# Optimization experiments

Hardware: AMD Instinct MI355X
Metric: run time of the kernel (lower is better)

## Reference

```python
import jax, jax.numpy as jnp
import numpy as np

B, IN, H = 8192, 1024, 1024

def setup_inputs() -> dict:
    key = jax.random.key(0)
    ks = jax.random.split(key, 11)
    s = 1.0 / np.sqrt(IN + H)  # torch Linear default init range
    def W(k):
        return jax.random.uniform(k, (H, IN + H), jnp.float32, -s, s)
    def b(k):
        return jax.random.uniform(k, (H,), jnp.float32, -s, s)
    return {
        "inputs": jax.random.normal(ks[0], (B, IN), jnp.float32),
        "hidden": jax.random.normal(ks[1], (B, H), jnp.float32),
        "c": jax.random.normal(ks[2], (B, H), jnp.float32),
        "Wf": W(ks[3]), "bf": b(ks[4]),
        "Wi": W(ks[5]), "bi": b(ks[6]),
        "Wo": W(ks[7]), "bo": b(ks[8]),
        "Wc": W(ks[9]), "bc": b(ks[10]),
    }

def reference(inputs, hidden, c, Wf, bf, Wi, bi, Wo, bo, Wc, bc):
    # concat order matches torch: [hidden, inputs]
    x = jnp.concatenate([hidden, inputs], axis=1)  # [B, H+IN]
    # fuse the four gate linears into one GEMM: [B, H+IN] x [H+IN, 4H]
    Wall = jnp.concatenate([Wf, Wi, Wo, Wc], axis=0)  # [4H, H+IN]
    ball = jnp.concatenate([bf, bi, bo, bc], axis=0)  # [4H]
    gates = x @ Wall.T + ball                         # [B, 4H]
    f, i, o, c_hat = jnp.split(gates, 4, axis=1)
    f = jax.nn.sigmoid(f)
    i = jax.nn.sigmoid(i)
    o = jax.nn.sigmoid(o)
    c_hat = jnp.tanh(c_hat)
    c_new = f * c + i * c_hat
    h_new = o * jnp.tanh(c_new)
    return (h_new, c_new)
```

## Files before the change

### kernel.cpp

```cpp
#include <hip/hip_runtime.h>
#include <cstdint>

#define Bdim 8192
#define Hdim 1024
#define Kdim 2048
#define BM 128
#define BU 64

#define XELEMS ((size_t)Bdim * Kdim)
#define WELEMS ((size_t)4 * Hdim * Kdim)
#define WGATE  ((size_t)Hdim * Kdim)

typedef __bf16 bf16;
typedef bf16  bf16x8   __attribute__((ext_vector_type(8)));
typedef float floatx16 __attribute__((ext_vector_type(16)));

typedef __attribute__((address_space(1))) uint32_t gu32;
typedef __attribute__((address_space(3))) uint32_t lu32;

__device__ __forceinline__ void gl_lds16(const bf16* g, bf16* l) {
    __builtin_amdgcn_global_load_lds((gu32*)(bf16*)g, (lu32*)l, 16, 0, 0);
}

__device__ __forceinline__ float sigf(float x) {
    return 1.0f / (1.0f + __expf(-x));
}
__device__ __forceinline__ float tanhfast(float x) {
    return 2.0f / (1.0f + __expf(-2.0f * x)) - 1.0f;
}

__global__ __launch_bounds__(256) void cvt_kernel(
    const float* __restrict__ inp, const float* __restrict__ hid,
    const float* __restrict__ Wf,  const float* __restrict__ Wi,
    const float* __restrict__ Wo,  const float* __restrict__ Wc,
    bf16* __restrict__ xc, bf16* __restrict__ wc)
{
    const size_t id = (size_t)blockIdx.x * 256 + threadIdx.x;
    const size_t e  = id * 8;
    const float* src;
    bf16* dst;
    if (e < XELEMS) {
        const size_t b = e >> 11;
        const size_t k = e & (Kdim - 1);
        src = (k < Hdim) ? (hid + b * Hdim + k) : (inp + b * Hdim + (k - Hdim));
        dst = xc + e;
    } else {
        const size_t w = e - XELEMS;
        const size_t g = w >> 21;
        const float* Ws = (g == 0) ? Wf : (g == 1) ? Wi : (g == 2) ? Wo : Wc;
        src = Ws + (w & (WGATE - 1));
        dst = wc + w;
    }
    const float4 a  = *reinterpret_cast<const float4*>(src);
    const float4 b4 = *reinterpret_cast<const float4*>(src + 4);
    bf16x8 o;
    o[0] = (bf16)a.x;  o[1] = (bf16)a.y;  o[2] = (bf16)a.z;  o[3] = (bf16)a.w;
    o[4] = (bf16)b4.x; o[5] = (bf16)b4.y; o[6] = (bf16)b4.z; o[7] = (bf16)b4.w;
    *reinterpret_cast<bf16x8*>(dst) = o;
}

__global__ __launch_bounds__(256, 2) void lstm_fused(
    const bf16* __restrict__ xc,   const bf16* __restrict__ wc,
    const float* __restrict__ cin,
    const float* __restrict__ bfv, const float* __restrict__ biv,
    const float* __restrict__ bov, const float* __restrict__ bcv,
    float* __restrict__ out)
{
    __shared__ __align__(16) bf16 As[2 * BM * 32];
    __shared__ __align__(16) bf16 Bs[2 * 4 * BU * 32];

    const int tid  = threadIdx.x;
    const int lane = tid & 63;
    const int wv   = tid >> 6;
    const int m31  = lane & 31;
    const int h32  = lane >> 5;

    const int m0 = blockIdx.x * BM;
    const int u0 = blockIdx.y * BU;

    const bf16* gA[2];
    bf16* lA[2];
    #pragma unroll
    for (int c = 0; c < 2; ++c) {
        const int li   = c * 256 + tid;
        const int row  = li >> 2;
        const int slot = li & 3;
        const int gch  = slot ^ ((row >> 1) & 3);
        gA[c] = xc + (size_t)(m0 + row) * Kdim + gch * 8;
        lA[c] = &As[li * 8];
    }
    const bf16* gB[4];
    bf16* lB[4];
    #pragma unroll
    for (int c = 0; c < 4; ++c) {
        const int li   = c * 256 + tid;
        const int nr   = li >> 2;
        const int slot = li & 3;
        const int gch  = slot ^ ((nr >> 1) & 3);
        const int g    = nr >> 6;
        const int ul   = nr & 63;
        gB[c] = wc + (size_t)g * WGATE + (size_t)(u0 + ul) * Kdim + gch * 8;
        lB[c] = &Bs[li * 8];
    }

    const int rbase = (wv & 1) * 64;
    const int ubase = (wv >> 1) * 32;
    int aoff[2][2];
    #pragma unroll
    for (int a = 0; a < 2; ++a) {
        const int ra = rbase + a * 32 + m31;
        const int t  = (ra >> 1) & 3;
        #pragma unroll
        for (int ks = 0; ks < 2; ++ks)
            aoff[a][ks] = ra * 32 + (((ks * 2 + h32) ^ t) * 8);
    }
    int boff[4][2];
    #pragma unroll
    for (int g = 0; g < 4; ++g) {
        const int rb = g * 64 + ubase + m31;
        const int t  = (rb >> 1) & 3;
        #pragma unroll
        for (int ks = 0; ks < 2; ++ks)
            boff[g][ks] = rb * 32 + (((ks * 2 + h32) ^ t) * 8);
    }

    floatx16 acc[2][4] = {};

    for (int k0 = 0; k0 < Kdim; k0 += 64) {
        #pragma unroll
        for (int s = 0; s < 2; ++s) {
            const int kk = k0 + s * 32;
            gl_lds16(gA[0] + kk, lA[0] + s * (BM * 32));
            gl_lds16(gA[1] + kk, lA[1] + s * (BM * 32));
            gl_lds16(gB[0] + kk, lB[0] + s * (4 * BU * 32));
            gl_lds16(gB[1] + kk, lB[1] + s * (4 * BU * 32));
            gl_lds16(gB[2] + kk, lB[2] + s * (4 * BU * 32));
            gl_lds16(gB[3] + kk, lB[3] + s * (4 * BU * 32));
        }
        __syncthreads();

        #pragma unroll
        for (int s = 0; s < 2; ++s) {
            const bf16* Ab = As + s * (BM * 32);
            const bf16* Bb = Bs + s * (4 * BU * 32);
            bf16x8 af[2][2];
            #pragma unroll
            for (int a = 0; a < 2; ++a)
                #pragma unroll
                for (int ks = 0; ks < 2; ++ks)
                    af[a][ks] = *reinterpret_cast<const bf16x8*>(Ab + aoff[a][ks]);
            bf16x8 bg[4][2];
            #pragma unroll
            for (int g = 0; g < 4; ++g)
                #pragma unroll
                for (int ks = 0; ks < 2; ++ks)
                    bg[g][ks] = *reinterpret_cast<const bf16x8*>(Bb + boff[g][ks]);

            #pragma unroll
            for (int ks = 0; ks < 2; ++ks)
                #pragma unroll
                for (int a = 0; a < 2; ++a)
                    #pragma unroll
                    for (int g = 0; g < 4; ++g)
                        acc[a][g] = __builtin_amdgcn_mfma_f32_32x32x16_bf16(
                            af[a][ks], bg[g][ks], acc[a][g], 0, 0, 0);
        }
        __syncthreads();
    }

    const int m_base = m0 + rbase + 4 * h32;
    const int unit   = u0 + ubase + m31;
    const float bff = bfv[unit];
    const float bii = biv[unit];
    const float boo = bov[unit];
    const float bcc = bcv[unit];
    #pragma unroll
    for (int a = 0; a < 2; ++a) {
        #pragma unroll
        for (int rg = 0; rg < 16; ++rg) {
            const int row = m_base + a * 32 + (rg & 3) + 8 * (rg >> 2);
            const size_t off = (size_t)row * Hdim + unit;
            const float fg = sigf(acc[a][0][rg] + bff);
            const float ig = sigf(acc[a][1][rg] + bii);
            const float og = sigf(acc[a][2][rg] + boo);
            const float ch = tanhfast(acc[a][3][rg] + bcc);
            const float cn = fg * cin[off] + ig * ch;
            const float hn = og * tanhfast(cn);
            out[off] = hn;
            out[(size_t)Bdim * Hdim + off] = cn;
        }
    }
}

extern "C" void kernel_launch(void* const* d_in, const int* in_sizes, int n_in,
                              void* d_out, int out_size, void* d_ws, size_t ws_size,
                              hipStream_t stream) {
    const float* inputs = (const float*)d_in[0];
    const float* hidden = (const float*)d_in[1];
    const float* cprev  = (const float*)d_in[2];
    const float* Wf     = (const float*)d_in[3];
    const float* bfp    = (const float*)d_in[4];
    const float* Wi     = (const float*)d_in[5];
    const float* bip    = (const float*)d_in[6];
    const float* Wo     = (const float*)d_in[7];
    const float* bop    = (const float*)d_in[8];
    const float* Wc     = (const float*)d_in[9];
    const float* bcp    = (const float*)d_in[10];
    float* out = (float*)d_out;

    const size_t need = (XELEMS + WELEMS) * sizeof(bf16);
    if (ws_size < need) return;
    bf16* xc = (bf16*)d_ws;
    bf16* wc = xc + XELEMS;

    const int cvt_blocks = (int)((XELEMS + WELEMS) / 8 / 256);
    cvt_kernel<<<dim3(cvt_blocks), dim3(256), 0, stream>>>(
        inputs, hidden, Wf, Wi, Wo, Wc, xc, wc);

    dim3 grid(Bdim / BM, Hdim / BU);
    lstm_fused<<<grid, dim3(256), 0, stream>>>(
        xc, wc, cprev, bfp, bip, bop, bcp, out);
}
```

Baseline: 334.5 us.

## Software-pipeline K loop with double-buffered slabs and vmcnt-based waits; change LDS swizzle

Restructures the GEMM main loop from a load-all-then-compute scheme (two slabs loaded, full sync, compute, sync) into a rolling double-buffer. The next slab's global-to-LDS loads are issued right after computing on the current buffer, and partial vmcnt waits plus raw barriers replace the full __syncthreads. The intent is to overlap global memory latency with MFMA work. It also changes the XOR swizzle function for LDS chunks, presumably to reduce bank conflicts. The risk is in the hand-coded waitcnt encodings and barrier placement, which could be mistuned or unsafe.

```diff
diff --git a/kernel.cpp b/kernel.cpp
--- a/kernel.cpp
+++ b/kernel.cpp
@@ -6,6 +6,10 @@
 #define Kdim 2048
 #define BM 128
 #define BU 64
+#define NSLAB (Kdim / 32)
+
+#define ASZ (BM * 32)
+#define BSZ (4 * BU * 32)
 
 #define XELEMS ((size_t)Bdim * Kdim)
 #define WELEMS ((size_t)4 * Hdim * Kdim)
@@ -27,6 +31,10 @@
 }
 __device__ __forceinline__ float tanhfast(float x) {
     return 2.0f / (1.0f + __expf(-2.0f * x)) - 1.0f;
+}
+
+__device__ __forceinline__ int fsw(int r) {
+    return (((r >> 1) & 1) << 1) | ((r >> 2) & 1);
 }
 
 __global__ __launch_bounds__(256) void cvt_kernel(
@@ -66,8 +74,8 @@
     const float* __restrict__ bov, const float* __restrict__ bcv,
     float* __restrict__ out)
 {
-    __shared__ __align__(16) bf16 As[2 * BM * 32];
-    __shared__ __align__(16) bf16 Bs[2 * 4 * BU * 32];
+    __shared__ __align__(16) bf16 As[2 * ASZ];
+    __shared__ __align__(16) bf16 Bs[2 * BSZ];
 
     const int tid  = threadIdx.x;
     const int lane = tid & 63;
@@ -85,7 +93,7 @@
         const int li   = c * 256 + tid;
         const int row  = li >> 2;
         const int slot = li & 3;
-        const int gch  = slot ^ ((row >> 1) & 3);
+        const int gch  = slot ^ fsw(row);
         gA[c] = xc + (size_t)(m0 + row) * Kdim + gch * 8;
         lA[c] = &As[li * 8];
     }
@@ -96,7 +104,7 @@
         const int li   = c * 256 + tid;
         const int nr   = li >> 2;
         const int slot = li & 3;
-        const int gch  = slot ^ ((nr >> 1) & 3);
+        const int gch  = slot ^ fsw(nr);
         const int g    = nr >> 6;
         const int ul   = nr & 63;
         gB[c] = wc + (size_t)g * WGATE + (size_t)(u0 + ul) * Kdim + gch * 8;
@@ -109,63 +117,72 @@
     #pragma unroll
     for (int a = 0; a < 2; ++a) {
         const int ra = rbase + a * 32 + m31;
-        const int t  = (ra >> 1) & 3;
         #pragma unroll
         for (int ks = 0; ks < 2; ++ks)
-            aoff[a][ks] = ra * 32 + (((ks * 2 + h32) ^ t) * 8);
+            aoff[a][ks] = ra * 32 + (((ks * 2 + h32) ^ fsw(ra)) * 8);
     }
     int boff[4][2];
     #pragma unroll
     for (int g = 0; g < 4; ++g) {
         const int rb = g * 64 + ubase + m31;
-        const int t  = (rb >> 1) & 3;
         #pragma unroll
         for (int ks = 0; ks < 2; ++ks)
-            boff[g][ks] = rb * 32 + (((ks * 2 + h32) ^ t) * 8);
+            boff[g][ks] = rb * 32 + (((ks * 2 + h32) ^ fsw(rb)) * 8);
     }
 
     floatx16 acc[2][4] = {};
 
-    for (int k0 = 0; k0 < Kdim; k0 += 64) {
-        #pragma unroll
-        for (int s = 0; s < 2; ++s) {
-            const int kk = k0 + s * 32;
-            gl_lds16(gA[0] + kk, lA[0] + s * (BM * 32));
-            gl_lds16(gA[1] + kk, lA[1] + s * (BM * 32));
-            gl_lds16(gB[0] + kk, lB[0] + s * (4 * BU * 32));
-            gl_lds16(gB[1] + kk, lB[1] + s * (4 * BU * 32));
-            gl_lds16(gB[2] + kk, lB[2] + s * (4 * BU * 32));
-            gl_lds16(gB[3] + kk, lB[3] + s * (4 * BU * 32));
-        }
-        __syncthreads();
-
-        #pragma unroll
-        for (int s = 0; s < 2; ++s) {
-            const bf16* Ab = As + s * (BM * 32);
-            const bf16* Bb = Bs + s * (4 * BU * 32);
-            bf16x8 af[2][2];
+    #pragma unroll
+    for (int s = 0; s < 2; ++s) {
+        const int kk = s * 32;
+        gl_lds16(gA[0] + kk, lA[0] + s * ASZ);
+        gl_lds16(gA[1] + kk, lA[1] + s * ASZ);
+        gl_lds16(gB[0] + kk, lB[0] + s * BSZ);
+        gl_lds16(gB[1] + kk, lB[1] + s * BSZ);
+        gl_lds16(gB[2] + kk, lB[2] + s * BSZ);
+        gl_lds16(gB[3] + kk, lB[3] + s * BSZ);
+    }
+
+    for (int s = 0; s < NSLAB; ++s) {
+        if (s == NSLAB - 1) __builtin_amdgcn_s_waitcnt(0xF70);
+        else                __builtin_amdgcn_s_waitcnt(0xF76);
+        __builtin_amdgcn_s_barrier();
+
+        const int sel = s & 1;
+        const bf16* Ab = As + sel * ASZ;
+        const bf16* Bb = Bs + sel * BSZ;
+        bf16x8 af[2][2];
+        #pragma unroll
+        for (int a = 0; a < 2; ++a)
+            #pragma unroll
+            for (int ks = 0; ks < 2; ++ks)
+                af[a][ks] = *reinterpret_cast<const bf16x8*>(Ab + aoff[a][ks]);
+        bf16x8 bg[4][2];
+        #pragma unroll
+        for (int g = 0; g < 4; ++g)
+            #pragma unroll
+            for (int ks = 0; ks < 2; ++ks)
+                bg[g][ks] = *reinterpret_cast<const bf16x8*>(Bb + boff[g][ks]);
+
+        #pragma unroll
+        for (int ks = 0; ks < 2; ++ks)
             #pragma unroll
             for (int a = 0; a < 2; ++a)
                 #pragma unroll
-                for (int ks = 0; ks < 2; ++ks)
-                    af[a][ks] = *reinterpret_cast<const bf16x8*>(Ab + aoff[a][ks]);
-            bf16x8 bg[4][2];
-            #pragma unroll
-            for (int g = 0; g < 4; ++g)
-                #pragma unroll
-                for (int ks = 0; ks < 2; ++ks)
-                    bg[g][ks] = *reinterpret_cast<const bf16x8*>(Bb + boff[g][ks]);
-
-            #pragma unroll
-            for (int ks = 0; ks < 2; ++ks)
-                #pragma unroll
-                for (int a = 0; a < 2; ++a)
-                    #pragma unroll
-                    for (int g = 0; g < 4; ++g)
-                        acc[a][g] = __builtin_amdgcn_mfma_f32_32x32x16_bf16(
-                            af[a][ks], bg[g][ks], acc[a][g], 0, 0, 0);
+                for (int g = 0; g < 4; ++g)
+                    acc[a][g] = __builtin_amdgcn_mfma_f32_32x32x16_bf16(
+                        af[a][ks], bg[g][ks], acc[a][g], 0, 0, 0);
+
+        if (s + 2 < NSLAB) {
+            __builtin_amdgcn_s_barrier();
+            const int kk = (s + 2) * 32;
+            gl_lds16(gA[0] + kk, lA[0] + sel * ASZ);
+            gl_lds16(gA[1] + kk, lA[1] + sel * ASZ);
+            gl_lds16(gB[0] + kk, lB[0] + sel * BSZ);
+            gl_lds16(gB[1] + kk, lB[1] + sel * BSZ);
+            gl_lds16(gB[2] + kk, lB[2] + sel * BSZ);
+            gl_lds16(gB[3] + kk, lB[3] + sel * BSZ);
         }
-        __syncthreads();
     }
 
     const int m_base = m0 + rbase + 4 * h32;
```

Measured after the change: 335.0 us. No clear change (+0.1%).
